# Optimization experiments

Measured on AMD Instinct MI355X. Metric: run time of the kernel, lower is better.

The kernel has to match this reference:

```python
import jax, jax.numpy as jnp
import numpy as np

B, S, F = 512, 512, 128   # batch, seq_len, facts_size (= querry_size)
H1, H2 = 80, 40
PAD = float(-2**32 + 1)


def setup_inputs() -> dict:
    key = jax.random.key(0)
    ks = jax.random.split(key, 12)
    inp = {
        "query": jax.random.normal(ks[0], (B, F), jnp.float32),
        "facts": jax.random.normal(ks[1], (B, S, F), jnp.float32),
        "mask": jax.random.randint(ks[2], (B, S), 0, 2, jnp.int32),
        # mlp1: querry_size -> facts_size
        "W1": jax.random.normal(ks[3], (F, F), jnp.float32) / np.sqrt(F),
        "b1": jnp.zeros((F,), jnp.float32),
        # PReLU alpha (per-feature, init zeros)
        "alpha": jnp.zeros((F,), jnp.float32),
        # mlp2: 4*F -> 80
        "W2": jax.random.normal(ks[4], (4 * F, H1), jnp.float32) / np.sqrt(4 * F),
        "b2": jnp.zeros((H1,), jnp.float32),
        # mlp3: 80 -> 40
        "W3": jax.random.normal(ks[5], (H1, H2), jnp.float32) / np.sqrt(H1),
        "b3": jnp.zeros((H2,), jnp.float32),
        # mlp4: 40 -> 1
        "W4": jax.random.normal(ks[6], (H2, 1), jnp.float32) / np.sqrt(H2),
        "b4": jnp.zeros((1,), jnp.float32),
    }
    return inp


def reference(query, facts, mask, W1, b1, alpha, W2, b2, W3, b3, W4, b4):
    # mlp1 + PReLU on the query
    q = query @ W1 + b1                                   # [B, F]
    q = jnp.where(q >= 0, q, alpha * q)                   # PReLU, alpha per-feature
    # broadcast query over sequence (tile+reshape in the original)
    qs = jnp.broadcast_to(q[:, None, :], (q.shape[0], S, F))  # [B, S, F]
    din = jnp.concatenate([qs, facts, qs - facts, qs * facts], axis=-1)  # [B,S,4F]
    h1 = jax.nn.sigmoid(din @ W2 + b2)                    # [B, S, 80]
    h2 = jax.nn.sigmoid(h1 @ W3 + b3)                     # [B, S, 40]
    scores = (h2 @ W4 + b4)[..., 0][:, None, :]           # [B, 1, S]
    key_masks = (mask == 1)[:, None, :]                   # [B, 1, S]
    scores = jnp.where(key_masks, scores, PAD)
    scores = jax.nn.softmax(scores, axis=-1)              # softmax over seq
    out = jnp.einsum("bqs,bsf->bqf", scores, facts)       # [B, 1, F]  (mode SUM)
    return out
```

## Files before the change

### kernel.cpp

```cpp
#include <hip/hip_runtime.h>
#include <hip/hip_bf16.h>

typedef __bf16 bf16x8 __attribute__((ext_vector_type(8)));
typedef float  f32x4  __attribute__((ext_vector_type(4)));

#define WBT_STRIDE 136
#define H1_STRIDE  104
#define W3T_STRIDE 104

#define LOAD_TILE(av, tile)                                                     \
    {                                                                           \
        const float* p0 = &fb[(size_t)(wave * 64 + (tile) * 16 + m) * 128 + qd * 8]; \
        _Pragma("unroll")                                                       \
        for (int kc = 0; kc < 4; ++kc) {                                        \
            av[kc][0] = *(const f32x4*)(p0 + kc * 32);                          \
            av[kc][1] = *(const f32x4*)(p0 + kc * 32 + 4);                      \
        }                                                                       \
    }

#define CONV_AF(af, av)                                                         \
    _Pragma("unroll")                                                           \
    for (int kc = 0; kc < 4; ++kc)                                              \
        _Pragma("unroll")                                                       \
        for (int i = 0; i < 8; ++i)                                             \
            af[kc][i] = (__bf16)((i < 4) ? av[kc][0][i] : av[kc][1][i - 4]);

#define SCORE_TILE(af, mvv, tile)                                               \
    {                                                                           \
         \
        _Pragma("unroll")                                                       \
        for (int ct = 0; ct < 5; ++ct) {                                        \
            f32x4 acc = {0.f, 0.f, 0.f, 0.f};                                   \
            _Pragma("unroll")                                                   \
            for (int kc = 0; kc < 4; ++kc) {                                    \
                bf16x8 bfr = *(const bf16x8*)&WbT[(ct * 16 + m) * WBT_STRIDE + kc * 32 + qd * 8]; \
                acc = __builtin_amdgcn_mfma_f32_16x16x32_bf16(af[kc], bfr, acc, 0, 0, 0); \
            }                                                                   \
            const int col = ct * 16 + m;    \
            const float qc = qcs[col];                                          \
            _Pragma("unroll")                                                   \
            for (int r = 0; r < 4; ++r) {                                       \
                float x = acc[r] + qc;                                          \
                float h = __builtin_amdgcn_rcpf(1.0f + __expf(-x));             \
                h1w[(qd * 4 + r) * H1_STRIDE + col] = (__bf16)h;                \
            }                                                                   \
        }                                                                       \
        asm volatile("s_waitcnt lgkmcnt(0)" ::: "memory");    \
                      \
        bf16x8 a2[3];                                                           \
        _Pragma("unroll")                                                       \
        for (int kc = 0; kc < 3; ++kc)                                          \
            a2[kc] = *(const bf16x8*)&h1w[m * H1_STRIDE + kc * 32 + qd * 8];    \
        float sc[4] = {0.f, 0.f, 0.f, 0.f};                                     \
        _Pragma("unroll")                                                       \
        for (int ct = 0; ct < 3; ++ct) {                                        \
            f32x4 acc2 = {0.f, 0.f, 0.f, 0.f};                                  \
            _Pragma("unroll")                                                   \
            for (int kc = 0; kc < 3; ++kc) {                                    \
                bf16x8 bfr = *(const bf16x8*)&W3T[(ct * 16 + m) * W3T_STRIDE + kc * 32 + qd * 8]; \
                acc2 = __builtin_amdgcn_mfma_f32_16x16x32_bf16(a2[kc], bfr, acc2, 0, 0, 0); \
            }                                                                   \
            const int col = ct * 16 + m;                                        \
            const float w4v = w4s[col], b3v = b3s[col];                         \
            _Pragma("unroll")                                                   \
            for (int r = 0; r < 4; ++r) {                                       \
                float h2 = __builtin_amdgcn_rcpf(1.0f + __expf(-(acc2[r] + b3v))); \
                sc[r] = fmaf(h2, w4v, sc[r]);                                   \
            }                                                                   \
        }                                                                       \
        _Pragma("unroll")                                                       \
        for (int d = 1; d < 16; d <<= 1)                                        \
            _Pragma("unroll")                                                   \
            for (int r = 0; r < 4; ++r)                                         \
                sc[r] += __shfl_xor(sc[r], d);                                  \
          \
        float s0v = __int_as_float(__builtin_amdgcn_ds_bpermute(idx, __float_as_int(sc[0]))); \
        float s1v = __int_as_float(__builtin_amdgcn_ds_bpermute(idx, __float_as_int(sc[1]))); \
        float s2v = __int_as_float(__builtin_amdgcn_ds_bpermute(idx, __float_as_int(sc[2]))); \
        float s3v = __int_as_float(__builtin_amdgcn_ds_bpermute(idx, __float_as_int(sc[3]))); \
        const int rr = m & 3;                                                   \
        float srow = (rr == 0) ? s0v : (rr == 1) ? s1v : (rr == 2) ? s2v : s3v; \
               \
        const float pmv = ((mvv) == 1) ? __expf(srow) : 0.f;                    \
        Zl += pmv;                                                              \
        if (qd == 0) pmall[wave * 64 + (tile) * 16 + m] = pmv;                  \
    }

__global__ __launch_bounds__(512, 2)
void attn_fused(const float* __restrict__ query,
                const float* __restrict__ facts,
                const int*   __restrict__ mask,
                const float* __restrict__ W1, const float* __restrict__ b1,
                const float* __restrict__ alpha,
                const float* __restrict__ W2, const float* __restrict__ b2,
                const float* __restrict__ W3, const float* __restrict__ b3,
                const float* __restrict__ W4,
                float* __restrict__ out)
{
    __shared__ __align__(16) __bf16 WbT[80 * WBT_STRIDE];
    __shared__ __align__(16) __bf16 W3T[48 * W3T_STRIDE];
    __shared__ __align__(16) __bf16 h1all[128 * H1_STRIDE];
    __shared__ float qy[128], qs[128], qcs[80];
    __shared__ float qpart[4][128], qcp[4][80];
    __shared__ float w4s[48], b3s[48];
    __shared__ float outw[8 * 128];
    __shared__ float pmall[8 * 64];
    __shared__ float Zw[8];

    const int b = blockIdx.x, t = threadIdx.x;
    const int wave = t >> 6, lane = t & 63, qd = lane >> 4, m = lane & 15;
    const float* fb = facts + (size_t)b * (512 * 128);
    const int*   mb = mask + b * 512;

    f32x4 av[4][2];
    LOAD_TILE(av, 0)
    const int mv0 = mb[wave * 64 + m];
    const int mv1 = mb[wave * 64 + 16 + m];
    const int mv2 = mb[wave * 64 + 32 + m];
    const int mv3 = mb[wave * 64 + 48 + m];

    if (t < 128) qy[t] = query[b * 128 + t];
    for (int e = t; e < 48 * 96; e += 512) {
        int j = e / 96, k = e % 96;
        W3T[j * W3T_STRIDE + k] = (j < 40 && k < 80) ? (__bf16)W3[k * 40 + j]
                                                     : (__bf16)0.0f;
    }
    for (int e = t; e < 128 * 16; e += 512) {
        int r = e >> 4, c = 80 + (e & 15);
        h1all[r * H1_STRIDE + c] = (__bf16)0.0f;
    }
    if (t < 48) { w4s[t] = (t < 40) ? W4[t] : 0.f; b3s[t] = (t < 40) ? b3[t] : 0.f; }
    __syncthreads();

    {
        int j = t & 127, kh = t >> 7;
        float acc = (kh == 0) ? b1[j] : 0.f;
        const float* w1p = W1 + (kh * 32) * 128 + j;
        #pragma unroll 8
        for (int k = 0; k < 32; ++k) acc = fmaf(qy[kh * 32 + k], w1p[k * 128], acc);
        qpart[kh][j] = acc;
    }
    __syncthreads();
    if (t < 128) {
        float s = (qpart[0][t] + qpart[1][t]) + (qpart[2][t] + qpart[3][t]);
        qs[t] = (s >= 0.f) ? s : alpha[t] * s;
    }
    __syncthreads();

    if (t < 320) {
        int jj = t % 80, hh = t / 80;
        float acc = (hh == 0) ? b2[jj] : 0.f;
        #pragma unroll 8
        for (int k = hh * 32; k < hh * 32 + 32; ++k)
            acc = fmaf(qs[k], W2[k * 80 + jj] + W2[(256 + k) * 80 + jj], acc);
        qcp[hh][jj] = acc;
    }
    for (int e = t; e < 128 * 80; e += 512) {
        int k = e / 80, n = e - k * 80;
        float w = W2[(128 + k) * 80 + n] - W2[(256 + k) * 80 + n]
                + qs[k] * W2[(384 + k) * 80 + n];
        WbT[n * WBT_STRIDE + k] = (__bf16)w;
    }
    __syncthreads();
    if (t < 80) qcs[t] = (qcp[0][t] + qcp[1][t]) + (qcp[2][t] + qcp[3][t]);
    __syncthreads();

    __bf16* h1w = &h1all[wave * 16 * H1_STRIDE];
    const int idx = ((((m >> 2) << 4) | m) << 2);

    float Zl = 0.f;
    bf16x8 af[4];

    CONV_AF(af, av)
    LOAD_TILE(av, 1)
    SCORE_TILE(af, mv0, 0)

    CONV_AF(af, av)
    LOAD_TILE(av, 2)
    SCORE_TILE(af, mv1, 1)

    CONV_AF(af, av)
    LOAD_TILE(av, 3)
    SCORE_TILE(af, mv2, 2)

    CONV_AF(af, av)
    SCORE_TILE(af, mv3, 3)

    asm volatile("s_waitcnt lgkmcnt(0)" ::: "memory");
    float oA = 0.f, oB = 0.f;
    {
        const float* fw = fb + (size_t)(wave * 64) * 128;
        const float* pmw = &pmall[wave * 64];
        #pragma unroll 8
        for (int s = 0; s < 64; ++s) {
            const float p = pmw[s];
            oA = fmaf(p, fw[s * 128 + lane], oA);
            oB = fmaf(p, fw[s * 128 + 64 + lane], oB);
        }
        outw[wave * 128 + lane] = oA;
        outw[wave * 128 + 64 + lane] = oB;
    }

    #pragma unroll
    for (int d = 1; d < 16; d <<= 1) Zl += __shfl_xor(Zl, d);
    if (lane == 0) Zw[wave] = Zl;
    __syncthreads();

    if (t < 128) {
        float v = 0.f, Z = 0.f;
        #pragma unroll
        for (int w = 0; w < 8; ++w) { v += outw[w * 128 + t]; Z += Zw[w]; }
        out[b * 128 + t] = v / Z;
    }
}

extern "C" void kernel_launch(void* const* d_in, const int* in_sizes, int n_in,
                              void* d_out, int out_size, void* d_ws, size_t ws_size,
                              hipStream_t stream) {
    (void)in_sizes; (void)n_in; (void)d_ws; (void)ws_size; (void)out_size;
    const float* query = (const float*)d_in[0];
    const float* facts = (const float*)d_in[1];
    const int*   mask  = (const int*)d_in[2];
    const float* W1 = (const float*)d_in[3];
    const float* b1 = (const float*)d_in[4];
    const float* al = (const float*)d_in[5];
    const float* W2 = (const float*)d_in[6];
    const float* b2 = (const float*)d_in[7];
    const float* W3 = (const float*)d_in[8];
    const float* b3 = (const float*)d_in[9];
    const float* W4 = (const float*)d_in[10];
    const float* b4 = (const float*)d_in[11];
    (void)b4;
    attn_fused<<<dim3(512), dim3(512), 0, stream>>>(
        query, facts, mask, W1, b1, al, W2, b2, W3, b3, W4, (float*)d_out);
}
```

Baseline: 228.4 us.

## Compact masked-in sequence rows per wave and skip fully masked tiles

Each wave ballots its 64 mask values, builds a compacted list of active row indices in shared memory, and gathers only those rows of facts for the MFMA scoring and the weighted sum. Tiles of 16 that hold no active rows are skipped, which with a random mask removes roughly half the scoring math and facts reads. The cost is gathered row loads instead of contiguous ones, extra shared-memory index traffic, and data-dependent branching that can leave waves with different amounts of work.

```diff
diff --git a/kernel.cpp b/kernel.cpp
--- a/kernel.cpp
+++ b/kernel.cpp
@@ -8,9 +8,9 @@
 #define H1_STRIDE  104
 #define W3T_STRIDE 104
 
-#define LOAD_TILE(av, tile)                                                     \
+#define LOAD_CT(av, rl)                                                         \
     {                                                                           \
-        const float* p0 = &fb[(size_t)(wave * 64 + (tile) * 16 + m) * 128 + qd * 8]; \
+        const float* p0 = &fb[(size_t)(wave * 64 + (rl)) * 128 + qd * 8];       \
         _Pragma("unroll")                                                       \
         for (int kc = 0; kc < 4; ++kc) {                                        \
             av[kc][0] = *(const f32x4*)(p0 + kc * 32);                          \
@@ -25,7 +25,7 @@
         for (int i = 0; i < 8; ++i)                                             \
             af[kc][i] = (__bf16)((i < 4) ? av[kc][0][i] : av[kc][1][i - 4]);
 
-#define SCORE_TILE(af, mvv, tile)                                               \
+#define SCORE_CT(af, tile)                                                      \
     {                                                                           \
          \
         _Pragma("unroll")                                                       \
@@ -80,8 +80,7 @@
         float s3v = __int_as_float(__builtin_amdgcn_ds_bpermute(idx, __float_as_int(sc[3]))); \
         const int rr = m & 3;                                                   \
         float srow = (rr == 0) ? s0v : (rr == 1) ? s1v : (rr == 2) ? s2v : s3v; \
-               \
-        const float pmv = ((mvv) == 1) ? __expf(srow) : 0.f;                    \
+        const float pmv = (((tile) * 16 + m) < cnt) ? __expf(srow) : 0.f;       \
         Zl += pmv;                                                              \
         if (qd == 0) pmall[wave * 64 + (tile) * 16 + m] = pmv;                  \
     }
@@ -105,6 +104,7 @@
     __shared__ float w4s[48], b3s[48];
     __shared__ float outw[8 * 128];
     __shared__ float pmall[8 * 64];
+    __shared__ unsigned char cidx8[8 * 64];
     __shared__ float Zw[8];
 
     const int b = blockIdx.x, t = threadIdx.x;
@@ -112,12 +112,23 @@
     const float* fb = facts + (size_t)b * (512 * 128);
     const int*   mb = mask + b * 512;
 
+    const int mvl = mb[wave * 64 + lane];
+    const unsigned long long bal = __ballot(mvl == 1);
+    const int cnt = __popcll(bal);
+    cidx8[wave * 64 + lane] = 0;
+    asm volatile("s_waitcnt lgkmcnt(0)" ::: "memory");
+    if (mvl == 1) {
+        const int rank = __popcll(bal & ((1ull << lane) - 1ull));
+        cidx8[wave * 64 + rank] = (unsigned char)lane;
+    }
+    asm volatile("s_waitcnt lgkmcnt(0)" ::: "memory");
+    const int rl0 = cidx8[wave * 64 +  0 + m];
+    const int rl1 = cidx8[wave * 64 + 16 + m];
+    const int rl2 = cidx8[wave * 64 + 32 + m];
+    const int rl3 = cidx8[wave * 64 + 48 + m];
+
     f32x4 av[4][2];
-    LOAD_TILE(av, 0)
-    const int mv0 = mb[wave * 64 + m];
-    const int mv1 = mb[wave * 64 + 16 + m];
-    const int mv2 = mb[wave * 64 + 32 + m];
-    const int mv3 = mb[wave * 64 + 48 + m];
+    LOAD_CT(av, rl0)
 
     if (t < 128) qy[t] = query[b * 128 + t];
     for (int e = t; e < 48 * 96; e += 512) {
@@ -172,30 +183,35 @@
     bf16x8 af[4];
 
     CONV_AF(af, av)
-    LOAD_TILE(av, 1)
-    SCORE_TILE(af, mv0, 0)
-
-    CONV_AF(af, av)
-    LOAD_TILE(av, 2)
-    SCORE_TILE(af, mv1, 1)
-
-    CONV_AF(af, av)
-    LOAD_TILE(av, 3)
-    SCORE_TILE(af, mv2, 2)
-
-    CONV_AF(af, av)
-    SCORE_TILE(af, mv3, 3)
+    if (cnt > 16) LOAD_CT(av, rl1)
+    SCORE_CT(af, 0)
+    if (cnt > 16) {
+        CONV_AF(af, av)
+        if (cnt > 32) LOAD_CT(av, rl2)
+        SCORE_CT(af, 1)
+    }
+    if (cnt > 32) {
+        CONV_AF(af, av)
+        if (cnt > 48) LOAD_CT(av, rl3)
+        SCORE_CT(af, 2)
+    }
+    if (cnt > 48) {
+        CONV_AF(af, av)
+        SCORE_CT(af, 3)
+    }
 
     asm volatile("s_waitcnt lgkmcnt(0)" ::: "memory");
     float oA = 0.f, oB = 0.f;
     {
         const float* fw = fb + (size_t)(wave * 64) * 128;
         const float* pmw = &pmall[wave * 64];
-        #pragma unroll 8
-        for (int s = 0; s < 64; ++s) {
-            const float p = pmw[s];
-            oA = fmaf(p, fw[s * 128 + lane], oA);
-            oB = fmaf(p, fw[s * 128 + 64 + lane], oB);
+        const unsigned char* ci = &cidx8[wave * 64];
+        #pragma unroll 4
+        for (int j = 0; j < cnt; ++j) {
+            const float p = pmw[j];
+            const int rl = ci[j];
+            oA = fmaf(p, fw[rl * 128 + lane], oA);
+            oB = fmaf(p, fw[rl * 128 + 64 + lane], oB);
         }
         outw[wave * 128 + lane] = oA;
         outw[wave * 128 + 64 + lane] = oB;
```

After: 219.3 us. 1.04x faster.
